# Optimization experiments

Measured on AMD Instinct MI355X. Metric: run time of the kernel, lower is better.

## Reference

```python
import jax, jax.numpy as jnp
import numpy as np

NEG_INF = -1e9  # same masked_fill constant as the torch module
ALPHA = 0.1     # LeakyReLU negative slope


def setup_inputs() -> dict:
    key = jax.random.key(0)
    k1, k2, k3, k4, k5 = jax.random.split(key, 5)
    B, N, Din, Dout = 8, 2048, 512, 512
    features = jax.random.normal(k1, (B, N, Din), dtype=jnp.float32)
    graph = jax.random.randint(k2, (B, N, N), 0, 2, dtype=jnp.int64)
    # xavier_uniform with gain=1.414: limit = gain*sqrt(6/(fan_in+fan_out))
    lim_w = 1.414 * np.sqrt(6.0 / (Din + Dout))
    w = jax.random.uniform(k3, (Din, Dout), jnp.float32, -lim_w, lim_w)
    lim_a = 1.414 * np.sqrt(6.0 / (Dout + 1))
    a1 = jax.random.uniform(k4, (Dout, 1), jnp.float32, -lim_a, lim_a)
    a2 = jax.random.uniform(k5, (Dout, 1), jnp.float32, -lim_a, lim_a)
    return {"features": features, "graph": graph, "w": w, "a1": a1, "a2": a2}


def reference(features, graph, w, a1, a2):
    # hidden: [B, N, Dout]
    hidden = jnp.einsum("bni,io->bno", features, w)
    s1 = hidden @ a1  # [B, N, 1] -> broadcasts over columns
    s2 = hidden @ a2  # [B, N, 1] -> transposed broadcasts over rows
    # e[b,i,j] = leaky_relu(s1[b,i] + s2[b,j])
    e = jax.nn.leaky_relu(s1 + jnp.swapaxes(s2, 1, 2), negative_slope=ALPHA)
    e = jnp.where(graph == 0, NEG_INF, e)
    attn = jax.nn.softmax(e, axis=-1)  # [B, N, N]; dropout p=0 -> identity
    h_prime = jnp.einsum("bij,bjo->bio", attn, hidden)
    return jax.nn.elu(h_prime)  # concat=True
```

## Files before the change

kernel.cpp:

```cpp
#include <hip/hip_runtime.h>
#include <math.h>

#define B_ 8
#define N_ 2048
#define D_ 512
#define NROWS (B_ * N_)
#define NEG_ALPHA 0.1f

typedef __bf16 bf16;
typedef __bf16 bf16x4 __attribute__((ext_vector_type(4)));
typedef __bf16 bf16x8 __attribute__((ext_vector_type(8)));
typedef float f32x4 __attribute__((ext_vector_type(4)));
typedef float f32x16 __attribute__((ext_vector_type(16)));

#define HTB_BATCH ((D_ / 32) * (N_ / 16) * 512)

__global__ __launch_bounds__(256) void k_prep(const float* __restrict__ W,
                                              bf16* __restrict__ Wt) {
  __shared__ float tile[64][65];
  const int din0 = blockIdx.y * 64, dout0 = blockIdx.x * 64;
  const int tx = threadIdx.x & 63, tg = threadIdx.x >> 6;
#pragma unroll
  for (int rr = 0; rr < 16; ++rr) {
    int dr = tg * 16 + rr;
    tile[dr][tx] = W[(size_t)(din0 + dr) * D_ + dout0 + tx];
  }
  __syncthreads();
#pragma unroll
  for (int rr = 0; rr < 4; ++rr) {
    int dl = rr * 16 + (threadIdx.x >> 4);
    int nl = (threadIdx.x & 15) * 4;
    bf16x4 v = {(bf16)tile[nl][dl], (bf16)tile[nl + 1][dl],
                (bf16)tile[nl + 2][dl], (bf16)tile[nl + 3][dl]};
    *(bf16x4*)&Wt[(size_t)(dout0 + dl) * D_ + din0 + nl] = v;
  }
}

__global__ __launch_bounds__(256) void k_wa(const float* __restrict__ W,
                                            const float* __restrict__ a1,
                                            const float* __restrict__ a2,
                                            float* __restrict__ wa1,
                                            float* __restrict__ wa2) {
  const int wv = threadIdx.x >> 6, lane = threadIdx.x & 63;
  const int row = blockIdx.x * 4 + wv;
  const float* wr = W + (size_t)row * D_;
  float d1 = 0.f, d2 = 0.f;
#pragma unroll
  for (int p = 0; p < 8; ++p) {
    int c = lane + p * 64;
    float w = wr[c];
    d1 = fmaf(w, a1[c], d1);
    d2 = fmaf(w, a2[c], d2);
  }
#pragma unroll
  for (int off = 32; off > 0; off >>= 1) {
    d1 += __shfl_down(d1, off, 64);
    d2 += __shfl_down(d2, off, 64);
  }
  if (lane == 0) {
    wa1[row] = d1;
    wa2[row] = d2;
  }
}

__global__ __launch_bounds__(256) void k_scores_x(const float* __restrict__ X,
                                                  const float* __restrict__ wa1,
                                                  const float* __restrict__ wa2,
                                                  float* __restrict__ s1,
                                                  float* __restrict__ s2,
                                                  bf16* __restrict__ Xb) {
  const int wv = threadIdx.x >> 6, lane = threadIdx.x & 63;
  const int r = blockIdx.x * 4 + wv;
  const float* x = X + (size_t)r * D_;
  float d1 = 0.f, d2 = 0.f;
#pragma unroll
  for (int p = 0; p < 2; ++p) {
    int c = lane * 4 + p * 256;
    float4 xv = *(const float4*)&x[c];
    float4 w1 = *(const float4*)&wa1[c];
    float4 w2 = *(const float4*)&wa2[c];
    d1 += xv.x * w1.x + xv.y * w1.y + xv.z * w1.z + xv.w * w1.w;
    d2 += xv.x * w2.x + xv.y * w2.y + xv.z * w2.z + xv.w * w2.w;
    bf16x4 h = {(bf16)xv.x, (bf16)xv.y, (bf16)xv.z, (bf16)xv.w};
    *(bf16x4*)&Xb[(size_t)r * D_ + c] = h;
  }
#pragma unroll
  for (int off = 32; off > 0; off >>= 1) {
    d1 += __shfl_down(d1, off, 64);
    d2 += __shfl_down(d2, off, 64);
  }
  if (lane == 0) {
    s1[r] = d1;
    s2[r] = d2;
  }
}

__global__ __launch_bounds__(256) void k_gpack(const int* __restrict__ G,
                                               unsigned int* __restrict__ GB) {
  const size_t g = (size_t)blockIdx.x * 256 + threadIdx.x;
  const int* src = G + g * 32;
  unsigned int bits = 0;
#pragma unroll
  for (int p = 0; p < 8; ++p) {
    int4 v = *(const int4*)&src[p * 4];
    bits |= (unsigned)(v.x != 0) << (p * 4);
    bits |= (unsigned)(v.y != 0) << (p * 4 + 1);
    bits |= (unsigned)(v.z != 0) << (p * 4 + 2);
    bits |= (unsigned)(v.w != 0) << (p * 4 + 3);
  }
  GB[g] = bits;
}

#define LDH 40

__global__ __launch_bounds__(256, 2) void k_hiddenT(const bf16* __restrict__ Xb,
                                                    const bf16* __restrict__ Wt,
                                                    bf16* __restrict__ HtB) {
  __shared__ bf16 As[128][LDH];
  __shared__ bf16 Bs[128][LDH];
  const int t = threadIdx.x;
  const int m0 = blockIdx.y * 128;
  const int n0 = blockIdx.x * 128;
  const int lane = t & 63, w = t >> 6;
  const int wm = w >> 1, wn = w & 1;
  const int l15 = lane & 15, q = lane >> 4;

  f32x4 acc[4][4];
#pragma unroll
  for (int i = 0; i < 4; ++i)
#pragma unroll
    for (int j = 0; j < 4; ++j) acc[i][j] = (f32x4){0.f, 0.f, 0.f, 0.f};

  bf16x8 av[2], bv[2];
#pragma unroll
  for (int p = 0; p < 2; ++p) {
    int s = t + p * 256;
    av[p] = *(const bf16x8*)&Wt[(size_t)(m0 + (s >> 2)) * D_ + (s & 3) * 8];
    bv[p] = *(const bf16x8*)&Xb[(size_t)(n0 + (s >> 2)) * D_ + (s & 3) * 8];
  }

  for (int k0 = 0; k0 < D_; k0 += 32) {
    __syncthreads();
#pragma unroll
    for (int p = 0; p < 2; ++p) {
      int s = t + p * 256;
      *(bf16x8*)&As[s >> 2][(s & 3) * 8] = av[p];
      *(bf16x8*)&Bs[s >> 2][(s & 3) * 8] = bv[p];
    }
    __syncthreads();
    if (k0 + 32 < D_) {
#pragma unroll
      for (int p = 0; p < 2; ++p) {
        int s = t + p * 256;
        av[p] = *(const bf16x8*)&Wt[(size_t)(m0 + (s >> 2)) * D_ + k0 + 32 + (s & 3) * 8];
        bv[p] = *(const bf16x8*)&Xb[(size_t)(n0 + (s >> 2)) * D_ + k0 + 32 + (s & 3) * 8];
      }
    }
    bf16x8 a[4], bb[4];
#pragma unroll
    for (int i = 0; i < 4; ++i)
      a[i] = *(const bf16x8*)&As[wm * 64 + i * 16 + l15][q * 8];
#pragma unroll
    for (int j = 0; j < 4; ++j)
      bb[j] = *(const bf16x8*)&Bs[wn * 64 + j * 16 + l15][q * 8];
#pragma unroll
    for (int i = 0; i < 4; ++i)
#pragma unroll
      for (int j = 0; j < 4; ++j)
        acc[i][j] =
            __builtin_amdgcn_mfma_f32_16x16x32_bf16(a[i], bb[j], acc[i][j], 0, 0, 0);
  }
#pragma unroll
  for (int i = 0; i < 4; ++i)
#pragma unroll
    for (int r = 0; r < 4; ++r) {
      int dout = m0 + wm * 64 + i * 16 + q * 4 + r;
#pragma unroll
      for (int j = 0; j < 4; ++j) {
        int row = n0 + wn * 64 + j * 16 + l15;
        int bb_ = row >> 11;
        int jj = row & (N_ - 1);
        size_t addr = (size_t)bb_ * HTB_BATCH +
                      ((size_t)((dout >> 5) * (N_ / 16) + (jj >> 4)) * 64 +
                       ((jj >> 3) & 1) * 32 + (dout & 31)) *
                          8 +
                      (jj & 7);
        HtB[addr] = (bf16)acc[i][j][r];
      }
    }
}

#define AT_BM 64
#define AT_BK 64
#define LDP 72
#define NIT (N_ / AT_BK)
#define GROW 272

#define ATTN_BODY(PS, BC, BN, IT)                                              \
  {                                                                            \
    const int j0_ = (IT)*AT_BK;                                                \
    unsigned gbyte = gb_s[pi][(IT)*8 + (t & 7)];                               \
    float pv[8];                                                               \
    {                                                                          \
      f32x4 sA = *(const f32x4*)&s2s[j0_ + pj];                                \
      f32x4 sB = *(const f32x4*)&s2s[j0_ + pj + 4];                            \
      float sv[8] = {sA.x, sA.y, sA.z, sA.w, sB.x, sB.y, sB.z, sB.w};          \
      _Pragma("unroll") for (int q_ = 0; q_ < 8; ++q_) {                       \
        float e = s1r + sv[q_];                                                \
        e = (e > 0.f) ? e : NEG_ALPHA * e;                                     \
        pv[q_] = ((gbyte >> q_) & 1) ? __expf(e) : 0.f;                        \
        rsum += pv[q_];                                                        \
      }                                                                        \
    }                                                                          \
    {                                                                          \
      bf16x8 pb = {(bf16)pv[0], (bf16)pv[1], (bf16)pv[2], (bf16)pv[3],         \
                   (bf16)pv[4], (bf16)pv[5], (bf16)pv[6], (bf16)pv[7]};        \
      *(bf16x8*)&Ps[PS][pi][pj] = pb;                                          \
    }                                                                          \
    __syncthreads();            \
    {               \
      int j0n = ((IT) + 1 < NIT) ? ((IT) + 1) * AT_BK : 0;                     \
      _Pragma("unroll") for (int nt = 0; nt < 2; ++nt)                         \
          _Pragma("unroll") for (int ks = 0; ks < 4; ++ks)                     \
              BN[nt][ks] = *(const bf16x8*)&Hb[(size_t)((                      \
                  ((w * 2 + nt) * (N_ / 16) + (j0n >> 4) + ks) * 64 + lane))   \
                  * 8];                                                        \
    }                                                                          \
    _Pragma("unroll") for (int ks = 0; ks < 4; ++ks) {                         \
      const int ko = ks * 16 + hf * 8;                                         \
      bf16x8 a0 = *(const bf16x8*)&Ps[PS][r31][ko];                            \
      bf16x8 a1 = *(const bf16x8*)&Ps[PS][32 + r31][ko];                       \
      acc[0][0] = __builtin_amdgcn_mfma_f32_32x32x16_bf16(a0, BC[0][ks],       \
                                                          acc[0][0], 0, 0, 0); \
      acc[0][1] = __builtin_amdgcn_mfma_f32_32x32x16_bf16(a0, BC[1][ks],       \
                                                          acc[0][1], 0, 0, 0); \
      acc[1][0] = __builtin_amdgcn_mfma_f32_32x32x16_bf16(a1, BC[0][ks],       \
                                                          acc[1][0], 0, 0, 0); \
      acc[1][1] = __builtin_amdgcn_mfma_f32_32x32x16_bf16(a1, BC[1][ks],       \
                                                          acc[1][1], 0, 0, 0); \
    }                                                                          \
  }

__global__ __launch_bounds__(512) void k_attn(const bf16* __restrict__ HtB,
                                              const unsigned char* __restrict__ GB,
                                              const float* __restrict__ s1,
                                              const float* __restrict__ s2,
                                              float* __restrict__ out) {
  __shared__ __align__(16) bf16 Ps[2][AT_BM][LDP];
  __shared__ float s2s[N_];
  __shared__ __align__(16) unsigned char gb_s[AT_BM][GROW];
  __shared__ float sum_part[AT_BM][8];
  __shared__ float row_sum[AT_BM];

  const int t = threadIdx.x;
  const int bid = blockIdx.x;
  const int b = bid & 7;
  const int i0 = (bid >> 3) * AT_BM;
  const int lane = t & 63, w = t >> 6;
  const int r31 = lane & 31, hf = lane >> 5;

  const bf16* Hb = HtB + (size_t)b * HTB_BATCH;
  const unsigned char* GBb = GB + ((size_t)b * N_ + i0) * (N_ / 8);

  for (int c = t; c < N_; c += 512) s2s[c] = s2[b * N_ + c];
  {
    int gr = t >> 3, gc = (t & 7) * 32;
    int4 w0 = *(const int4*)&GBb[(size_t)gr * (N_ / 8) + gc];
    int4 w1 = *(const int4*)&GBb[(size_t)gr * (N_ / 8) + gc + 16];
    *(int4*)&gb_s[gr][gc] = w0;
    *(int4*)&gb_s[gr][gc + 16] = w1;
  }

  const int pi = t >> 3;
  const int pj = (t & 7) * 8;
  const float s1r = s1[b * N_ + i0 + pi];
  float rsum = 0.f;

  f32x16 acc[2][2];
#pragma unroll
  for (int i = 0; i < 2; ++i)
#pragma unroll
    for (int j = 0; j < 2; ++j)
#pragma unroll
      for (int r = 0; r < 16; ++r) acc[i][j][r] = 0.f;

  bf16x8 bA[2][4], bB[2][4];
#pragma unroll
  for (int nt = 0; nt < 2; ++nt)
#pragma unroll
    for (int ks = 0; ks < 4; ++ks)
      bA[nt][ks] = *(const bf16x8*)&Hb[(size_t)(
          ((w * 2 + nt) * (N_ / 16) + ks) * 64 + lane) * 8];

  __syncthreads();

#pragma unroll 1
  for (int i2 = 0; i2 < NIT / 2; ++i2) {
    const int it0 = i2 * 2;
    ATTN_BODY(0, bA, bB, it0);
    ATTN_BODY(1, bB, bA, it0 + 1);
  }

  sum_part[pi][t & 7] = rsum;
  __syncthreads();
  if (t < AT_BM) {
    float s = 0.f;
#pragma unroll
    for (int k = 0; k < 8; ++k) s += sum_part[t][k];
    row_sum[t] = s;
  }
  __syncthreads();

#pragma unroll
  for (int mt = 0; mt < 2; ++mt) {
    float inv[16];
#pragma unroll
    for (int r = 0; r < 16; ++r)
      inv[r] = 1.f / row_sum[mt * 32 + (r & 3) + 8 * (r >> 2) + 4 * hf];
#pragma unroll
    for (int nt = 0; nt < 2; ++nt) {
      const int d = w * 64 + nt * 32 + r31;
#pragma unroll
      for (int r = 0; r < 16; ++r) {
        int i = mt * 32 + (r & 3) + 8 * (r >> 2) + 4 * hf;
        float x = acc[mt][nt][r] * inv[r];
        out[((size_t)b * N_ + i0 + i) * D_ + d] = (x > 0.f) ? x : expm1f(x);
      }
    }
  }
}

extern "C" void kernel_launch(void* const* d_in, const int* in_sizes, int n_in,
                              void* d_out, int out_size, void* d_ws,
                              size_t ws_size, hipStream_t stream) {
  const float* X = (const float*)d_in[0];
  const int* graph = (const int*)d_in[1];
  const float* W = (const float*)d_in[2];
  const float* a1 = (const float*)d_in[3];
  const float* a2 = (const float*)d_in[4];
  float* out = (float*)d_out;

  char* ws = (char*)d_ws;
  bf16* Wt = (bf16*)ws;
  bf16* HtB = (bf16*)(ws + (1 << 19));
  bf16* Xb = (bf16*)(ws + (1 << 19) + (16 << 20));
  unsigned int* GBw = (unsigned int*)(ws + (1 << 19) + (32 << 20));
  float* s1 = (float*)(ws + (1 << 19) + (37 << 20));
  float* s2 = s1 + NROWS;
  float* wa1 = s2 + NROWS;
  float* wa2 = wa1 + D_;

  hipLaunchKernelGGL(k_prep, dim3(8, 8), dim3(256), 0, stream, W, Wt);
  hipLaunchKernelGGL(k_wa, dim3(128), dim3(256), 0, stream, W, a1, a2, wa1, wa2);
  hipLaunchKernelGGL(k_scores_x, dim3(NROWS / 4), dim3(256), 0, stream, X, wa1,
                     wa2, s1, s2, Xb);
  hipLaunchKernelGGL(k_gpack, dim3((B_ * N_ * N_) / (256 * 32)), dim3(256), 0,
                     stream, graph, GBw);
  hipLaunchKernelGGL(k_hiddenT, dim3(NROWS / 128, D_ / 128), dim3(256), 0,
                     stream, Xb, Wt, HtB);
  hipLaunchKernelGGL(k_attn, dim3(N_ / AT_BM * B_), dim3(512), 0, stream, HtB,
                     (const unsigned char*)GBw, s1, s2, out);
}
```

Baseline: 299.3 us.

## Fuse graph packing into score kernel, use LDS direct loads, split attention over D

Three separate changes. The graph bit-packing is merged into the score/cast kernel, which removes one launch and lets the two streaming passes share a grid; the grids match (4096 blocks × 256 threads cover 2^20 words). The hidden GEMM now stages tiles with global_load_lds direct-to-LDS copies into unpadded shared arrays and raises the occupancy hint, at the cost of dropping register prefetch and possibly adding bank conflicts. The attention kernel is split across two halves of the output dimension, doubling the block count with half the accumulators per wave, but each half recomputes the softmax probabilities and rereads the mask.

Result: no change. 304.2 us (+1.6%).

```diff
diff --git a/kernel.cpp b/kernel.cpp
--- a/kernel.cpp
+++ b/kernel.cpp
@@ -68,7 +68,9 @@
                                                   const float* __restrict__ wa2,
                                                   float* __restrict__ s1,
                                                   float* __restrict__ s2,
-                                                  bf16* __restrict__ Xb) {
+                                                  bf16* __restrict__ Xb,
+                                                  const int* __restrict__ G,
+                                                  unsigned int* __restrict__ GB) {
   const int wv = threadIdx.x >> 6, lane = threadIdx.x & 63;
   const int r = blockIdx.x * 4 + wv;
   const float* x = X + (size_t)r * D_;
@@ -84,6 +86,20 @@
     bf16x4 h = {(bf16)xv.x, (bf16)xv.y, (bf16)xv.z, (bf16)xv.w};
     *(bf16x4*)&Xb[(size_t)r * D_ + c] = h;
   }
+  {
+    const size_t g = (size_t)blockIdx.x * 256 + threadIdx.x;
+    const int* src = G + g * 32;
+    unsigned int bits = 0;
+#pragma unroll
+    for (int p = 0; p < 8; ++p) {
+      int4 v = *(const int4*)&src[p * 4];
+      bits |= (unsigned)(v.x != 0) << (p * 4);
+      bits |= (unsigned)(v.y != 0) << (p * 4 + 1);
+      bits |= (unsigned)(v.z != 0) << (p * 4 + 2);
+      bits |= (unsigned)(v.w != 0) << (p * 4 + 3);
+    }
+    GB[g] = bits;
+  }
 #pragma unroll
   for (int off = 32; off > 0; off >>= 1) {
     d1 += __shfl_down(d1, off, 64);
@@ -95,29 +111,11 @@
   }
 }
 
-__global__ __launch_bounds__(256) void k_gpack(const int* __restrict__ G,
-                                               unsigned int* __restrict__ GB) {
-  const size_t g = (size_t)blockIdx.x * 256 + threadIdx.x;
-  const int* src = G + g * 32;
-  unsigned int bits = 0;
-#pragma unroll
-  for (int p = 0; p < 8; ++p) {
-    int4 v = *(const int4*)&src[p * 4];
-    bits |= (unsigned)(v.x != 0) << (p * 4);
-    bits |= (unsigned)(v.y != 0) << (p * 4 + 1);
-    bits |= (unsigned)(v.z != 0) << (p * 4 + 2);
-    bits |= (unsigned)(v.w != 0) << (p * 4 + 3);
-  }
-  GB[g] = bits;
-}
-
-#define LDH 40
-
-__global__ __launch_bounds__(256, 2) void k_hiddenT(const bf16* __restrict__ Xb,
+__global__ __launch_bounds__(256, 3) void k_hiddenT(const bf16* __restrict__ Xb,
                                                     const bf16* __restrict__ Wt,
                                                     bf16* __restrict__ HtB) {
-  __shared__ bf16 As[128][LDH];
-  __shared__ bf16 Bs[128][LDH];
+  __shared__ bf16 As[128 * 32];
+  __shared__ bf16 Bs[128 * 32];
   const int t = threadIdx.x;
   const int m0 = blockIdx.y * 128;
   const int n0 = blockIdx.x * 128;
@@ -131,44 +129,39 @@
 #pragma unroll
     for (int j = 0; j < 4; ++j) acc[i][j] = (f32x4){0.f, 0.f, 0.f, 0.f};
 
-  bf16x8 av[2], bv[2];
-#pragma unroll
-  for (int p = 0; p < 2; ++p) {
-    int s = t + p * 256;
-    av[p] = *(const bf16x8*)&Wt[(size_t)(m0 + (s >> 2)) * D_ + (s & 3) * 8];
-    bv[p] = *(const bf16x8*)&Xb[(size_t)(n0 + (s >> 2)) * D_ + (s & 3) * 8];
-  }
+  const int srow = lane >> 2;
+  const int scol = (lane & 3) * 8;
 
   for (int k0 = 0; k0 < D_; k0 += 32) {
-    __syncthreads();
 #pragma unroll
     for (int p = 0; p < 2; ++p) {
-      int s = t + p * 256;
-      *(bf16x8*)&As[s >> 2][(s & 3) * 8] = av[p];
-      *(bf16x8*)&Bs[s >> 2][(s & 3) * 8] = bv[p];
+      const int row = w * 32 + p * 16 + srow;
+      const bf16* ga = &Wt[(size_t)(m0 + row) * D_ + k0 + scol];
+      const bf16* gb = &Xb[(size_t)(n0 + row) * D_ + k0 + scol];
+      __builtin_amdgcn_global_load_lds(
+          (const __attribute__((address_space(1))) void*)ga,
+          (__attribute__((address_space(3))) void*)&As[(w * 32 + p * 16) * 32],
+          16, 0, 0);
+      __builtin_amdgcn_global_load_lds(
+          (const __attribute__((address_space(1))) void*)gb,
+          (__attribute__((address_space(3))) void*)&Bs[(w * 32 + p * 16) * 32],
+          16, 0, 0);
     }
     __syncthreads();
-    if (k0 + 32 < D_) {
-#pragma unroll
-      for (int p = 0; p < 2; ++p) {
-        int s = t + p * 256;
-        av[p] = *(const bf16x8*)&Wt[(size_t)(m0 + (s >> 2)) * D_ + k0 + 32 + (s & 3) * 8];
-        bv[p] = *(const bf16x8*)&Xb[(size_t)(n0 + (s >> 2)) * D_ + k0 + 32 + (s & 3) * 8];
-      }
-    }
     bf16x8 a[4], bb[4];
 #pragma unroll
     for (int i = 0; i < 4; ++i)
-      a[i] = *(const bf16x8*)&As[wm * 64 + i * 16 + l15][q * 8];
+      a[i] = *(const bf16x8*)&As[(wm * 64 + i * 16 + l15) * 32 + q * 8];
 #pragma unroll
     for (int j = 0; j < 4; ++j)
-      bb[j] = *(const bf16x8*)&Bs[wn * 64 + j * 16 + l15][q * 8];
+      bb[j] = *(const bf16x8*)&Bs[(wn * 64 + j * 16 + l15) * 32 + q * 8];
 #pragma unroll
     for (int i = 0; i < 4; ++i)
 #pragma unroll
       for (int j = 0; j < 4; ++j)
         acc[i][j] =
             __builtin_amdgcn_mfma_f32_16x16x32_bf16(a[i], bb[j], acc[i][j], 0, 0, 0);
+    __syncthreads();
   }
 #pragma unroll
   for (int i = 0; i < 4; ++i)
@@ -220,24 +213,18 @@
     __syncthreads();            \
     {               \
       int j0n = ((IT) + 1 < NIT) ? ((IT) + 1) * AT_BK : 0;                     \
-      _Pragma("unroll") for (int nt = 0; nt < 2; ++nt)                         \
-          _Pragma("unroll") for (int ks = 0; ks < 4; ++ks)                     \
-              BN[nt][ks] = *(const bf16x8*)&Hb[(size_t)((                      \
-                  ((w * 2 + nt) * (N_ / 16) + (j0n >> 4) + ks) * 64 + lane))   \
-                  * 8];                                                        \
+      _Pragma("unroll") for (int ks = 0; ks < 4; ++ks)                         \
+          BN[ks] = *(const bf16x8*)&Hb[(size_t)((                              \
+              (dch * (N_ / 16) + (j0n >> 4) + ks) * 64 + lane)) * 8];          \
     }                                                                          \
     _Pragma("unroll") for (int ks = 0; ks < 4; ++ks) {                         \
       const int ko = ks * 16 + hf * 8;                                         \
       bf16x8 a0 = *(const bf16x8*)&Ps[PS][r31][ko];                            \
       bf16x8 a1 = *(const bf16x8*)&Ps[PS][32 + r31][ko];                       \
-      acc[0][0] = __builtin_amdgcn_mfma_f32_32x32x16_bf16(a0, BC[0][ks],       \
-                                                          acc[0][0], 0, 0, 0); \
-      acc[0][1] = __builtin_amdgcn_mfma_f32_32x32x16_bf16(a0, BC[1][ks],       \
-                                                          acc[0][1], 0, 0, 0); \
-      acc[1][0] = __builtin_amdgcn_mfma_f32_32x32x16_bf16(a1, BC[0][ks],       \
-                                                          acc[1][0], 0, 0, 0); \
-      acc[1][1] = __builtin_amdgcn_mfma_f32_32x32x16_bf16(a1, BC[1][ks],       \
-                                                          acc[1][1], 0, 0, 0); \
+      acc[0] = __builtin_amdgcn_mfma_f32_32x32x16_bf16(a0, BC[ks], acc[0],     \
+                                                       0, 0, 0);               \
+      acc[1] = __builtin_amdgcn_mfma_f32_32x32x16_bf16(a1, BC[ks], acc[1],     \
+                                                       0, 0, 0);               \
     }                                                                          \
   }
 
@@ -255,9 +242,11 @@
   const int t = threadIdx.x;
   const int bid = blockIdx.x;
   const int b = bid & 7;
-  const int i0 = (bid >> 3) * AT_BM;
+  const int i0 = ((bid >> 3) & 31) * AT_BM;
+  const int ds = bid >> 8;
   const int lane = t & 63, w = t >> 6;
   const int r31 = lane & 31, hf = lane >> 5;
+  const int dch = ds * 8 + w;
 
   const bf16* Hb = HtB + (size_t)b * HTB_BATCH;
   const unsigned char* GBb = GB + ((size_t)b * N_ + i0) * (N_ / 8);
@@ -276,21 +265,16 @@
   const float s1r = s1[b * N_ + i0 + pi];
   float rsum = 0.f;
 
-  f32x16 acc[2][2];
+  f32x16 acc[2];
 #pragma unroll
   for (int i = 0; i < 2; ++i)
 #pragma unroll
-    for (int j = 0; j < 2; ++j)
-#pragma unroll
-      for (int r = 0; r < 16; ++r) acc[i][j][r] = 0.f;
-
-  bf16x8 bA[2][4], bB[2][4];
-#pragma unroll
-  for (int nt = 0; nt < 2; ++nt)
-#pragma unroll
-    for (int ks = 0; ks < 4; ++ks)
-      bA[nt][ks] = *(const bf16x8*)&Hb[(size_t)(
-          ((w * 2 + nt) * (N_ / 16) + ks) * 64 + lane) * 8];
+    for (int r = 0; r < 16; ++r) acc[i][r] = 0.f;
+
+  bf16x8 bA[4], bB[4];
+#pragma unroll
+  for (int ks = 0; ks < 4; ++ks)
+    bA[ks] = *(const bf16x8*)&Hb[(size_t)((dch * (N_ / 16) + ks) * 64 + lane) * 8];
 
   __syncthreads();
 
@@ -317,15 +301,12 @@
 #pragma unroll
     for (int r = 0; r < 16; ++r)
       inv[r] = 1.f / row_sum[mt * 32 + (r & 3) + 8 * (r >> 2) + 4 * hf];
-#pragma unroll
-    for (int nt = 0; nt < 2; ++nt) {
-      const int d = w * 64 + nt * 32 + r31;
-#pragma unroll
-      for (int r = 0; r < 16; ++r) {
-        int i = mt * 32 + (r & 3) + 8 * (r >> 2) + 4 * hf;
-        float x = acc[mt][nt][r] * inv[r];
-        out[((size_t)b * N_ + i0 + i) * D_ + d] = (x > 0.f) ? x : expm1f(x);
-      }
+    const int d = ds * 256 + w * 32 + r31;
+#pragma unroll
+    for (int r = 0; r < 16; ++r) {
+      int i = mt * 32 + (r & 3) + 8 * (r >> 2) + 4 * hf;
+      float x = acc[mt][r] * inv[r];
+      out[((size_t)b * N_ + i0 + i) * D_ + d] = (x > 0.f) ? x : expm1f(x);
     }
   }
 }
@@ -353,11 +334,9 @@
   hipLaunchKernelGGL(k_prep, dim3(8, 8), dim3(256), 0, stream, W, Wt);
   hipLaunchKernelGGL(k_wa, dim3(128), dim3(256), 0, stream, W, a1, a2, wa1, wa2);
   hipLaunchKernelGGL(k_scores_x, dim3(NROWS / 4), dim3(256), 0, stream, X, wa1,
-                     wa2, s1, s2, Xb);
-  hipLaunchKernelGGL(k_gpack, dim3((B_ * N_ * N_) / (256 * 32)), dim3(256), 0,
-                     stream, graph, GBw);
+                     wa2, s1, s2, Xb, graph, GBw);
   hipLaunchKernelGGL(k_hiddenT, dim3(NROWS / 128, D_ / 128), dim3(256), 0,
                      stream, Xb, Wt, HtB);
-  hipLaunchKernelGGL(k_attn, dim3(N_ / AT_BM * B_), dim3(512), 0, stream, HtB,
-                     (const unsigned char*)GBw, s1, s2, out);
-}
+  hipLaunchKernelGGL(k_attn, dim3(N_ / AT_BM * B_ * 2), dim3(512), 0, stream,
+                     HtB, (const unsigned char*)GBw, s1, s2, out);
+}
```

## Fuse graph packing into score kernel, drop bf16 X copy, async-LDS attention loop

Applied to the files above, without the earlier changes.

The graph bit-packing moves into the score kernel, and the standalone k_gpack launch is removed. The hidden GEMM now reads fp32 X directly and converts it to bf16 while staging shared memory, so the intermediate Xb buffer and its global write/read are gone. The attention kernel switches to 32-wide K steps with H tiles streamed into double-buffered LDS via global_load_lds, and one barrier per iteration with explicit waitcnt control replaces the register-double-buffered loads. ELU now uses __expf(x)-1 instead of expm1f, which trades a little accuracy near zero for cheaper math.

Measured after the change: 308.9 us. 3.2% more time.

```diff
diff --git a/kernel.cpp b/kernel.cpp
--- a/kernel.cpp
+++ b/kernel.cpp
@@ -68,7 +68,8 @@
                                                   const float* __restrict__ wa2,
                                                   float* __restrict__ s1,
                                                   float* __restrict__ s2,
-                                                  bf16* __restrict__ Xb) {
+                                                  const int* __restrict__ G,
+                                                  unsigned int* __restrict__ GB) {
   const int wv = threadIdx.x >> 6, lane = threadIdx.x & 63;
   const int r = blockIdx.x * 4 + wv;
   const float* x = X + (size_t)r * D_;
@@ -81,8 +82,20 @@
     float4 w2 = *(const float4*)&wa2[c];
     d1 += xv.x * w1.x + xv.y * w1.y + xv.z * w1.z + xv.w * w1.w;
     d2 += xv.x * w2.x + xv.y * w2.y + xv.z * w2.z + xv.w * w2.w;
-    bf16x4 h = {(bf16)xv.x, (bf16)xv.y, (bf16)xv.z, (bf16)xv.w};
-    *(bf16x4*)&Xb[(size_t)r * D_ + c] = h;
+  }
+  {
+    const size_t g = (size_t)blockIdx.x * 256 + threadIdx.x;
+    const int* src = G + g * 32;
+    unsigned int bits = 0;
+#pragma unroll
+    for (int p = 0; p < 8; ++p) {
+      int4 v = *(const int4*)&src[p * 4];
+      bits |= (unsigned)(v.x != 0) << (p * 4);
+      bits |= (unsigned)(v.y != 0) << (p * 4 + 1);
+      bits |= (unsigned)(v.z != 0) << (p * 4 + 2);
+      bits |= (unsigned)(v.w != 0) << (p * 4 + 3);
+    }
+    GB[g] = bits;
   }
 #pragma unroll
   for (int off = 32; off > 0; off >>= 1) {
@@ -95,25 +108,9 @@
   }
 }
 
-__global__ __launch_bounds__(256) void k_gpack(const int* __restrict__ G,
-                                               unsigned int* __restrict__ GB) {
-  const size_t g = (size_t)blockIdx.x * 256 + threadIdx.x;
-  const int* src = G + g * 32;
-  unsigned int bits = 0;
-#pragma unroll
-  for (int p = 0; p < 8; ++p) {
-    int4 v = *(const int4*)&src[p * 4];
-    bits |= (unsigned)(v.x != 0) << (p * 4);
-    bits |= (unsigned)(v.y != 0) << (p * 4 + 1);
-    bits |= (unsigned)(v.z != 0) << (p * 4 + 2);
-    bits |= (unsigned)(v.w != 0) << (p * 4 + 3);
-  }
-  GB[g] = bits;
-}
-
 #define LDH 40
 
-__global__ __launch_bounds__(256, 2) void k_hiddenT(const bf16* __restrict__ Xb,
+__global__ __launch_bounds__(256, 2) void k_hiddenT(const float* __restrict__ X,
                                                     const bf16* __restrict__ Wt,
                                                     bf16* __restrict__ HtB) {
   __shared__ bf16 As[128][LDH];
@@ -131,12 +128,17 @@
 #pragma unroll
     for (int j = 0; j < 4; ++j) acc[i][j] = (f32x4){0.f, 0.f, 0.f, 0.f};
 
-  bf16x8 av[2], bv[2];
+  bf16x8 av[2];
+  float4 bv[4];
 #pragma unroll
   for (int p = 0; p < 2; ++p) {
     int s = t + p * 256;
     av[p] = *(const bf16x8*)&Wt[(size_t)(m0 + (s >> 2)) * D_ + (s & 3) * 8];
-    bv[p] = *(const bf16x8*)&Xb[(size_t)(n0 + (s >> 2)) * D_ + (s & 3) * 8];
+  }
+#pragma unroll
+  for (int p = 0; p < 4; ++p) {
+    int s = t + p * 256;
+    bv[p] = *(const float4*)&X[(size_t)(n0 + (s >> 3)) * D_ + (s & 7) * 4];
   }
 
   for (int k0 = 0; k0 < D_; k0 += 32) {
@@ -145,7 +147,13 @@
     for (int p = 0; p < 2; ++p) {
       int s = t + p * 256;
       *(bf16x8*)&As[s >> 2][(s & 3) * 8] = av[p];
-      *(bf16x8*)&Bs[s >> 2][(s & 3) * 8] = bv[p];
+    }
+#pragma unroll
+    for (int p = 0; p < 4; ++p) {
+      int s = t + p * 256;
+      float4 v = bv[p];
+      bf16x4 h = {(bf16)v.x, (bf16)v.y, (bf16)v.z, (bf16)v.w};
+      *(bf16x4*)&Bs[s >> 3][(s & 7) * 4] = h;
     }
     __syncthreads();
     if (k0 + 32 < D_) {
@@ -153,7 +161,11 @@
       for (int p = 0; p < 2; ++p) {
         int s = t + p * 256;
         av[p] = *(const bf16x8*)&Wt[(size_t)(m0 + (s >> 2)) * D_ + k0 + 32 + (s & 3) * 8];
-        bv[p] = *(const bf16x8*)&Xb[(size_t)(n0 + (s >> 2)) * D_ + k0 + 32 + (s & 3) * 8];
+      }
+#pragma unroll
+      for (int p = 0; p < 4; ++p) {
+        int s = t + p * 256;
+        bv[p] = *(const float4*)&X[(size_t)(n0 + (s >> 3)) * D_ + k0 + 32 + (s & 7) * 4];
       }
     }
     bf16x8 a[4], bb[4];
@@ -191,55 +203,10 @@
 }
 
 #define AT_BM 64
-#define AT_BK 64
-#define LDP 72
+#define AT_BK 32
+#define LDP 40
 #define NIT (N_ / AT_BK)
 #define GROW 272
-
-#define ATTN_BODY(PS, BC, BN, IT)                                              \
-  {                                                                            \
-    const int j0_ = (IT)*AT_BK;                                                \
-    unsigned gbyte = gb_s[pi][(IT)*8 + (t & 7)];                               \
-    float pv[8];                                                               \
-    {                                                                          \
-      f32x4 sA = *(const f32x4*)&s2s[j0_ + pj];                                \
-      f32x4 sB = *(const f32x4*)&s2s[j0_ + pj + 4];                            \
-      float sv[8] = {sA.x, sA.y, sA.z, sA.w, sB.x, sB.y, sB.z, sB.w};          \
-      _Pragma("unroll") for (int q_ = 0; q_ < 8; ++q_) {                       \
-        float e = s1r + sv[q_];                                                \
-        e = (e > 0.f) ? e : NEG_ALPHA * e;                                     \
-        pv[q_] = ((gbyte >> q_) & 1) ? __expf(e) : 0.f;                        \
-        rsum += pv[q_];                                                        \
-      }                                                                        \
-    }                                                                          \
-    {                                                                          \
-      bf16x8 pb = {(bf16)pv[0], (bf16)pv[1], (bf16)pv[2], (bf16)pv[3],         \
-                   (bf16)pv[4], (bf16)pv[5], (bf16)pv[6], (bf16)pv[7]};        \
-      *(bf16x8*)&Ps[PS][pi][pj] = pb;                                          \
-    }                                                                          \
-    __syncthreads();            \
-    {               \
-      int j0n = ((IT) + 1 < NIT) ? ((IT) + 1) * AT_BK : 0;                     \
-      _Pragma("unroll") for (int nt = 0; nt < 2; ++nt)                         \
-          _Pragma("unroll") for (int ks = 0; ks < 4; ++ks)                     \
-              BN[nt][ks] = *(const bf16x8*)&Hb[(size_t)((                      \
-                  ((w * 2 + nt) * (N_ / 16) + (j0n >> 4) + ks) * 64 + lane))   \
-                  * 8];                                                        \
-    }                                                                          \
-    _Pragma("unroll") for (int ks = 0; ks < 4; ++ks) {                         \
-      const int ko = ks * 16 + hf * 8;                                         \
-      bf16x8 a0 = *(const bf16x8*)&Ps[PS][r31][ko];                            \
-      bf16x8 a1 = *(const bf16x8*)&Ps[PS][32 + r31][ko];                       \
-      acc[0][0] = __builtin_amdgcn_mfma_f32_32x32x16_bf16(a0, BC[0][ks],       \
-                                                          acc[0][0], 0, 0, 0); \
-      acc[0][1] = __builtin_amdgcn_mfma_f32_32x32x16_bf16(a0, BC[1][ks],       \
-                                                          acc[0][1], 0, 0, 0); \
-      acc[1][0] = __builtin_amdgcn_mfma_f32_32x32x16_bf16(a1, BC[0][ks],       \
-                                                          acc[1][0], 0, 0, 0); \
-      acc[1][1] = __builtin_amdgcn_mfma_f32_32x32x16_bf16(a1, BC[1][ks],       \
-                                                          acc[1][1], 0, 0, 0); \
-    }                                                                          \
-  }
 
 __global__ __launch_bounds__(512) void k_attn(const bf16* __restrict__ HtB,
                                               const unsigned char* __restrict__ GB,
@@ -247,6 +214,7 @@
                                               const float* __restrict__ s2,
                                               float* __restrict__ out) {
   __shared__ __align__(16) bf16 Ps[2][AT_BM][LDP];
+  __shared__ __align__(16) bf16 Hs[2][16384];
   __shared__ float s2s[N_];
   __shared__ __align__(16) unsigned char gb_s[AT_BM][GROW];
   __shared__ float sum_part[AT_BM][8];
@@ -272,7 +240,8 @@
   }
 
   const int pi = t >> 3;
-  const int pj = (t & 7) * 8;
+  const int c8 = t & 7;
+  const int pj = c8 * 4;
   const float s1r = s1[b * N_ + i0 + pi];
   float rsum = 0.f;
 
@@ -284,24 +253,77 @@
 #pragma unroll
       for (int r = 0; r < 16; ++r) acc[i][j][r] = 0.f;
 
-  bf16x8 bA[2][4], bB[2][4];
+  bf16* HsF = &Hs[0][0];
 #pragma unroll
   for (int nt = 0; nt < 2; ++nt)
 #pragma unroll
-    for (int ks = 0; ks < 4; ++ks)
-      bA[nt][ks] = *(const bf16x8*)&Hb[(size_t)(
-          ((w * 2 + nt) * (N_ / 16) + ks) * 64 + lane) * 8];
+    for (int jo = 0; jo < 2; ++jo) {
+      const bf16* src =
+          &Hb[((size_t)(w * 2 + nt) * (N_ / 16) + jo) * 512 + lane * 8];
+      __builtin_amdgcn_global_load_lds(
+          (const __attribute__((address_space(1))) void*)src,
+          (__attribute__((address_space(3))) void*)
+              &HsF[w * 2048 + (nt * 2 + jo) * 512],
+          16, 0, 0);
+    }
 
   __syncthreads();
 
 #pragma unroll 1
-  for (int i2 = 0; i2 < NIT / 2; ++i2) {
-    const int it0 = i2 * 2;
-    ATTN_BODY(0, bA, bB, it0);
-    ATTN_BODY(1, bB, bA, it0 + 1);
-  }
-
-  sum_part[pi][t & 7] = rsum;
+  for (int it = 0; it < NIT; ++it) {
+    const int cur = it & 1;
+    {
+      unsigned gbits = (unsigned)(gb_s[pi][it * 4 + (c8 >> 1)]) >> ((c8 & 1) * 4);
+      f32x4 sv = *(const f32x4*)&s2s[it * AT_BK + pj];
+      float pv[4];
+#pragma unroll
+      for (int q_ = 0; q_ < 4; ++q_) {
+        float e = s1r + sv[q_];
+        e = (e > 0.f) ? e : NEG_ALPHA * e;
+        pv[q_] = ((gbits >> q_) & 1) ? __expf(e) : 0.f;
+        rsum += pv[q_];
+      }
+      bf16x4 pb = {(bf16)pv[0], (bf16)pv[1], (bf16)pv[2], (bf16)pv[3]};
+      *(bf16x4*)&Ps[cur][pi][pj] = pb;
+    }
+    {
+      const int jn = (it + 1 < NIT) ? it + 1 : 0;
+#pragma unroll
+      for (int nt = 0; nt < 2; ++nt)
+#pragma unroll
+        for (int jo = 0; jo < 2; ++jo) {
+          const bf16* src = &Hb[((size_t)(w * 2 + nt) * (N_ / 16) + jn * 2 + jo) *
+                                    512 +
+                                lane * 8];
+          __builtin_amdgcn_global_load_lds(
+              (const __attribute__((address_space(1))) void*)src,
+              (__attribute__((address_space(3))) void*)
+                  &HsF[(cur ^ 1) * 16384 + w * 2048 + (nt * 2 + jo) * 512],
+              16, 0, 0);
+        }
+    }
+    asm volatile("s_waitcnt lgkmcnt(0)" ::: "memory");
+    __builtin_amdgcn_sched_barrier(0);
+    __builtin_amdgcn_s_barrier();
+    __builtin_amdgcn_sched_barrier(0);
+    asm volatile("s_waitcnt vmcnt(4)" ::: "memory");
+    __builtin_amdgcn_sched_barrier(0);
+#pragma unroll
+    for (int ks = 0; ks < 2; ++ks) {
+      const int ko = ks * 16 + hf * 8;
+      bf16x8 a0 = *(const bf16x8*)&Ps[cur][r31][ko];
+      bf16x8 a1 = *(const bf16x8*)&Ps[cur][32 + r31][ko];
+      bf16x8 b0 = *(const bf16x8*)&HsF[cur * 16384 + w * 2048 + ks * 512 + lane * 8];
+      bf16x8 b1 =
+          *(const bf16x8*)&HsF[cur * 16384 + w * 2048 + (2 + ks) * 512 + lane * 8];
+      acc[0][0] = __builtin_amdgcn_mfma_f32_32x32x16_bf16(a0, b0, acc[0][0], 0, 0, 0);
+      acc[0][1] = __builtin_amdgcn_mfma_f32_32x32x16_bf16(a0, b1, acc[0][1], 0, 0, 0);
+      acc[1][0] = __builtin_amdgcn_mfma_f32_32x32x16_bf16(a1, b0, acc[1][0], 0, 0, 0);
+      acc[1][1] = __builtin_amdgcn_mfma_f32_32x32x16_bf16(a1, b1, acc[1][1], 0, 0, 0);
+    }
+  }
+
+  sum_part[pi][c8] = rsum;
   __syncthreads();
   if (t < AT_BM) {
     float s = 0.f;
@@ -324,7 +346,8 @@
       for (int r = 0; r < 16; ++r) {
         int i = mt * 32 + (r & 3) + 8 * (r >> 2) + 4 * hf;
         float x = acc[mt][nt][r] * inv[r];
-        out[((size_t)b * N_ + i0 + i) * D_ + d] = (x > 0.f) ? x : expm1f(x);
+        out[((size_t)b * N_ + i0 + i) * D_ + d] =
+            (x > 0.f) ? x : (__expf(x) - 1.f);
       }
     }
   }
@@ -343,9 +366,8 @@
   char* ws = (char*)d_ws;
   bf16* Wt = (bf16*)ws;
   bf16* HtB = (bf16*)(ws + (1 << 19));
-  bf16* Xb = (bf16*)(ws + (1 << 19) + (16 << 20));
-  unsigned int* GBw = (unsigned int*)(ws + (1 << 19) + (32 << 20));
-  float* s1 = (float*)(ws + (1 << 19) + (37 << 20));
+  unsigned int* GBw = (unsigned int*)(ws + (1 << 19) + (16 << 20));
+  float* s1 = (float*)(ws + (1 << 19) + (21 << 20));
   float* s2 = s1 + NROWS;
   float* wa1 = s2 + NROWS;
   float* wa2 = wa1 + D_;
@@ -353,11 +375,9 @@
   hipLaunchKernelGGL(k_prep, dim3(8, 8), dim3(256), 0, stream, W, Wt);
   hipLaunchKernelGGL(k_wa, dim3(128), dim3(256), 0, stream, W, a1, a2, wa1, wa2);
   hipLaunchKernelGGL(k_scores_x, dim3(NROWS / 4), dim3(256), 0, stream, X, wa1,
-                     wa2, s1, s2, Xb);
-  hipLaunchKernelGGL(k_gpack, dim3((B_ * N_ * N_) / (256 * 32)), dim3(256), 0,
-                     stream, graph, GBw);
+                     wa2, s1, s2, graph, GBw);
   hipLaunchKernelGGL(k_hiddenT, dim3(NROWS / 128, D_ / 128), dim3(256), 0,
-                     stream, Xb, Wt, HtB);
+                     stream, X, Wt, HtB);
   hipLaunchKernelGGL(k_attn, dim3(N_ / AT_BM * B_), dim3(512), 0, stream, HtB,
                      (const unsigned char*)GBw, s1, s2, out);
 }
```
